# Optimization experiments

Measured on AMD Instinct MI355X. Metric: run time of the kernel, lower is better.

## Reference

```python
import jax, jax.numpy as jnp
import numpy as np

B = 32
M = 3
MAG_DIM = 20
STD = 0.28
INV = float(1.0 / (np.sqrt(2.0) * STD))
NORM = float(1.0 / (np.sqrt(2.0 * np.pi) * STD))


def _lrelu(x):
    return jax.nn.leaky_relu(x, 0.01)


def _conv(x, w, b):
    y = jax.lax.conv_general_dilated(x, w, (2, 2), 'VALID',
                                     dimension_numbers=('NCHW', 'OIHW', 'NCHW'))
    return _lrelu(y + b[None, :, None, None])


def _combos(x):
    # x: [N, c, d] -> [N, c, c, 2d], pairs[n, i, j] = concat(x[n, i], x[n, j])
    # (matches torch getCombinations: tensorB = expand-over-i, tensorA = expand-over-j)
    N, c, d = x.shape
    left = jnp.broadcast_to(x[:, :, None, :], (N, c, c, d))
    right = jnp.broadcast_to(x[:, None, :, :], (N, c, c, d))
    return jnp.concatenate([left, right], axis=-1)


def _forward(batch, conv_w1, conv_b1, conv_w2, conv_b2, conv_w3, conv_b3, conv_w4, conv_b4,
             post_w, post_b, g_w1, g_b1, g_w2, g_b2, g_w3, g_b3, g_w4, g_b4,
             h_w1, h_b1, h_w2, h_b2, h_w3, h_b3, f_w1, f_b1, f_w2, f_b2, ff_w, ff_b):
    bsz = batch.shape[0]
    x = batch.reshape(bsz * 16, 1, 80, 80)
    # magnitude encoding (computed under no_grad in the original)
    mag = jnp.linspace(-1.0, 1.0, MAG_DIM).astype(batch.dtype)  # [20]
    t = jnp.tanh(x * (2.0 / 255.0) - 1.0)                        # [N,1,80,80]
    enc = NORM * jnp.exp(-(((t + mag[None, :, None, None]) * INV) ** 2))  # [N,20,80,80]
    enc = jax.lax.stop_gradient(enc)
    y = _conv(enc, conv_w1, conv_b1)   # [N,32,39,39]
    y = _conv(y, conv_w2, conv_b2)     # [N,32,19,19]
    y = _conv(y, conv_w3, conv_b3)     # [N,32,9,9]
    y = _conv(y, conv_w4, conv_b4)     # [N,32,4,4]
    obj = y.reshape(bsz * 16, 512) @ post_w + post_b             # [N,247]
    panel = obj.reshape(bsz, 16, 247)
    given, options = panel[:, :8], panel[:, 8:]
    giv = jnp.broadcast_to(given[:, None], (bsz, 8, 8, 247))
    ctx = jnp.concatenate([giv, options[:, :, None, :]], axis=2)  # [B,8,9,247]
    tags = jnp.broadcast_to(jnp.eye(9, dtype=batch.dtype), (bsz * 8, 9, 9))
    objects = jnp.concatenate([ctx.reshape(bsz * 8, 9, 247), tags], axis=-1)  # [B*8,9,256]

    z = _combos(objects).reshape(-1, 512)  # [B*8*81, 512]
    z = _lrelu(z @ g_w1 + g_b1)
    z = _lrelu(z @ g_w2 + g_b2)
    z = _lrelu(z @ g_w3 + g_b3)
    z = _lrelu(z @ g_w4 + g_b4)
    sum_j = z.reshape(bsz * 8, 9, 9, 256).sum(axis=2)  # [B*8,9,256]
    for i in range(h_w1.shape[0]):
        p = _combos(sum_j).reshape(-1, 512)
        z = _lrelu(p @ h_w1[i] + h_b1[i])
        z = _lrelu(z @ h_w2[i] + h_b2[i])
        z = _lrelu(z @ h_w3[i] + h_b3[i])
        sum_j = z.reshape(bsz * 8, 9, 9, 256).sum(axis=2)
    h_sum = sum_j.sum(axis=1)                          # [B*8,256]
    z = _lrelu(h_sum @ f_w1 + f_b1)
    z = _lrelu(z @ f_w2 + f_b2)
    result = z @ ff_w + ff_b                           # [B*8,1]
    answer = result.reshape(bsz, 8)
    loss = jnp.mean(h_sum ** 2) + jnp.mean(result ** 2)
    return answer, loss


def setup_inputs():
    key = jax.random.key(0)
    ks = iter(jax.random.split(key, 40))

    def U(shape, fan_in):
        s = 1.0 / np.sqrt(fan_in)
        return jax.random.uniform(next(ks), shape, jnp.float32, -s, s)

    inp = {
        'batch': jax.random.uniform(next(ks), (B, 16, 80, 80), jnp.float32, 0.0, 255.0),
        'conv_w1': U((32, MAG_DIM, 3, 3), MAG_DIM * 9), 'conv_b1': U((32,), MAG_DIM * 9),
        'conv_w2': U((32, 32, 3, 3), 288), 'conv_b2': U((32,), 288),
        'conv_w3': U((32, 32, 3, 3), 288), 'conv_b3': U((32,), 288),
        'conv_w4': U((32, 32, 3, 3), 288), 'conv_b4': U((32,), 288),
        'post_w': U((512, 247), 512), 'post_b': U((247,), 512),
        'g_w1': U((512, 512), 512), 'g_b1': U((512,), 512),
        'g_w2': U((512, 512), 512), 'g_b2': U((512,), 512),
        'g_w3': U((512, 512), 512), 'g_b3': U((512,), 512),
        'g_w4': U((512, 256), 512), 'g_b4': U((256,), 512),
        'h_w1': U((M, 512, 256), 512), 'h_b1': U((M, 256), 512),
        'h_w2': U((M, 256, 256), 256), 'h_b2': U((M, 256), 256),
        'h_w3': U((M, 256, 256), 256), 'h_b3': U((M, 256), 256),
        'f_w1': U((256, 256), 256), 'f_b1': U((256,), 256),
        'f_w2': U((256, 256), 256), 'f_b2': U((256,), 256),
        'ff_w': U((256, 1), 256), 'ff_b': U((1,), 256),
    }
    return inp


def reference(batch, conv_w1, conv_b1, conv_w2, conv_b2, conv_w3, conv_b3, conv_w4, conv_b4,
              post_w, post_b, g_w1, g_b1, g_w2, g_b2, g_w3, g_b3, g_w4, g_b4,
              h_w1, h_b1, h_w2, h_b2, h_w3, h_b3, f_w1, f_b1, f_w2, f_b2, ff_w, ff_b):
    return _forward(batch, conv_w1, conv_b1, conv_w2, conv_b2, conv_w3, conv_b3, conv_w4, conv_b4,
                    post_w, post_b, g_w1, g_b1, g_w2, g_b2, g_w3, g_b3, g_w4, g_b4,
                    h_w1, h_b1, h_w2, h_b2, h_w3, h_b3, f_w1, f_b1, f_w2, f_b2, ff_w, ff_b)
```

## Files before the change

kernel.cpp:

```cpp
#include <hip/hip_runtime.h>
#include <hip/hip_bf16.h>
#include <math.h>

static __device__ __forceinline__ float lrelu(float v){ return v > 0.0f ? v : 0.01f*v; }

static __device__ __forceinline__ unsigned short f2bf(float f){
  unsigned int u = __float_as_uint(f);
  unsigned int r = (u + 0x7fffu + ((u >> 16) & 1u)) >> 16;
  return (unsigned short)r;
}
static __device__ __forceinline__ float bf2f(unsigned short u){
  return __uint_as_float(((unsigned int)u) << 16);
}
static __device__ __forceinline__ unsigned int pack_bf2(float lo, float hi){
  __hip_bfloat162 bb = __float22bfloat162_rn(make_float2(lo, hi));
  return *reinterpret_cast<unsigned int*>(&bb);
}
static __device__ __forceinline__ void gload16(const void* g, void* l){
  __builtin_amdgcn_global_load_lds(
    (const __attribute__((address_space(1))) void*)(const void*)g,
    (__attribute__((address_space(3))) void*)l, 16, 0, 0);
}

#define ENC_NORM 1.4247939f
#define GC_C     6.3775511f
#define GC_2CD   1.3426423f
#define GC_CD2   0.070665395f
#define GC_S1    0.86820227f

typedef __attribute__((ext_vector_type(4))) float f32x4;
typedef __attribute__((ext_vector_type(8))) short bf16x8;

__global__ __launch_bounds__(256) void k_prep(
    const float* __restrict__ g_w1, const float* __restrict__ g_w2,
    const float* __restrict__ g_w3, const float* __restrict__ g_w4,
    const float* __restrict__ h_w1, const float* __restrict__ h_w2,
    const float* __restrict__ h_w3, const float* __restrict__ post_w,
    const float* __restrict__ conv_w2, const float* __restrict__ conv_w3,
    const float* __restrict__ conv_w4, const float* __restrict__ conv_w1,
    const float* __restrict__ f_w1, const float* __restrict__ f_w2,
    unsigned short* __restrict__ WT)
{
  int e = blockIdx.x*256 + threadIdx.x;
  float v;
  if (e < 262144) {
    int nn = e >> 8, kk = e & 255;
    v = (nn < 512) ? g_w1[kk*512 + nn] : g_w1[(256+kk)*512 + (nn-512)];
  } else if (e < 524288) {
    int r = e - 262144; int nn = r >> 9, kk = r & 511;
    v = g_w2[kk*512 + nn];
  } else if (e < 786432) {
    int r = e - 524288; int nn = r >> 9, kk = r & 511;
    v = g_w3[kk*512 + nn];
  } else if (e < 917504) {
    int r = e - 786432; int nn = r >> 9, kk = r & 511;
    v = g_w4[kk*256 + nn];
  } else if (e < 1310720) {
    int r = e - 917504; int i = r >> 17; int q = r & 131071;
    int nn = q >> 8, kk = q & 255;
    v = (nn < 256) ? h_w1[i*131072 + kk*256 + nn]
                   : h_w1[i*131072 + (256+kk)*256 + (nn-256)];
  } else if (e < 1507328) {
    int r = e - 1310720; int i = r >> 16; int q = r & 65535;
    int nn = q >> 8, kk = q & 255;
    v = h_w2[i*65536 + kk*256 + nn];
  } else if (e < 1703936) {
    int r = e - 1507328; int i = r >> 16; int q = r & 65535;
    int nn = q >> 8, kk = q & 255;
    v = h_w3[i*65536 + kk*256 + nn];
  } else if (e < 1835008) {
    int r = e - 1703936; int np = r >> 9, kp = r & 511;
    int px = kp >> 5, c = kp & 31;
    v = (np < 247) ? post_w[(c*16+px)*247 + np] : 0.f;
  } else if (e < 1862656) {
    int r = e - 1835008; int which = r / 9216; int q = r % 9216;
    int tap = q >> 10, o = (q >> 5) & 31, c = q & 31;
    const float* w = which==0 ? conv_w2 : (which==1 ? conv_w3 : conv_w4);
    v = w[(o*32+c)*9 + tap];
  } else if (e < 1871872) {
    int r = e - 1862656; int tap = r >> 10, o = (r >> 5) & 31, c = r & 31;
    v = (c < 20) ? conv_w1[(o*20+c)*9 + tap] : 0.f;
  } else if (e < 1937408) {
    int r = e - 1871872; int nn = r >> 8, kk = r & 255;
    v = f_w1[kk*256 + nn];
  } else {
    int r = e - 1937408; int nn = r >> 8, kk = r & 255;
    v = f_w2[kk*256 + nn];
  }
  WT[e] = f2bf(v);
}

__global__ __launch_bounds__(256, 1) void k_conv1m(
    const float* __restrict__ batch, const unsigned short* __restrict__ wc1,
    const float* __restrict__ bias, unsigned short* __restrict__ y)
{
  __shared__ unsigned short ench[7][41][40];
  int n = blockIdx.x;
  int h = blockIdx.y;
  int c0 = h * 40;
  int OWH = h ? 19 : 20;
  int owbase = h * 20;
  int tid = threadIdx.x;
  int lane = tid & 63, wid = tid >> 6;
  int lr = lane & 15, kg = lane >> 4;

  bf16x8 bf0[9], bf1[9];
  #pragma unroll
  for (int tap = 0; tap < 9; ++tap) {
    bf0[tap] = *(const bf16x8*)&wc1[tap*1024 + lr*32 + kg*8];
    bf1[tap] = *(const bf16x8*)&wc1[tap*1024 + (16+lr)*32 + kg*8];
  }
  float b0 = bias[lr], b1 = bias[16 + lr];
  const float S2 = GC_S1 * GC_S1;

  for (int s = 0; s < 13; ++s) {
    int orow0 = s * 3;
    int irow0 = orow0 * 2;
    const float* img = batch + (size_t)n*6400 + irow0*80;
    for (int p = tid; p < 7*41; p += 256) {
      int row = p / 41, hx = p % 41;
      int lc = (hx < 21) ? 2*hx : 2*(hx-21)+1;
      int c = c0 + lc;
      if (c > 78) continue;
      float x = img[row*80 + c];
      float E = __expf(x * (4.0f/255.0f) - 2.0f);
      float t = 1.0f - 2.0f*__builtin_amdgcn_rcpf(E + 1.0f);
      float z = t - 1.0f;
      float e = ENC_NORM * __expf(-GC_C*z*z);
      float rg = __expf(-GC_2CD*z - GC_CD2);
      unsigned int pk[16];
      #pragma unroll
      for (int cp = 0; cp < 10; ++cp) {
        float e1 = e * rg;
        pk[cp] = pack_bf2(e, e1);
        e  = e1 * rg * GC_S1;
        rg = rg * S2;
      }
      #pragma unroll
      for (int cp = 10; cp < 16; ++cp) pk[cp] = 0u;
      unsigned short* dst = &ench[row][hx][0];
      *(uint4*)(dst)      = *(uint4*)&pk[0];
      *(uint4*)(dst + 8)  = *(uint4*)&pk[4];
      *(uint4*)(dst + 16) = *(uint4*)&pk[8];
      *(uint4*)(dst + 24) = *(uint4*)&pk[12];
    }
    __syncthreads();

    int totpx = 3 * OWH;
    {
      int t = wid;
      int pa = t*16 + lr;
      int pc = (pa < totpx) ? pa : (totpx - 1);
      int ohl = pc / OWH, lw = pc % OWH;
      f32x4 acc0 = {0.f,0.f,0.f,0.f}, acc1 = {0.f,0.f,0.f,0.f};
      #pragma unroll
      for (int kh = 0; kh < 3; ++kh) {
        int r = ohl*2 + kh;
        #pragma unroll
        for (int kw = 0; kw < 3; ++kw) {
          int hidx = (kw == 1) ? (21 + lw) : (lw + (kw >> 1));
          bf16x8 a = *(const bf16x8*)&ench[r][hidx][kg*8];
          int tap = kh*3 + kw;
          acc0 = __builtin_amdgcn_mfma_f32_16x16x32_bf16(a, bf0[tap], acc0, 0, 0, 0);
          acc1 = __builtin_amdgcn_mfma_f32_16x16x32_bf16(a, bf1[tap], acc1, 0, 0, 0);
        }
      }
      #pragma unroll
      for (int rr = 0; rr < 4; ++rr) {
        int ps = t*16 + kg*4 + rr;
        if (ps < totpx) {
          int soh = orow0 + ps / OWH, sow = owbase + ps % OWH;
          unsigned short* op = y + (((size_t)n*39 + soh)*39 + sow)*32;
          op[lr]      = f2bf(lrelu(acc0[rr] + b0));
          op[16 + lr] = f2bf(lrelu(acc1[rr] + b1));
        }
      }
    }
    __syncthreads();
  }
}

template<int H, int W, int OH, int OW, int ROWS, int SLABS>
__global__ __launch_bounds__(256, 1) void k_cmfma(
    const unsigned short* __restrict__ in, const unsigned short* __restrict__ wc,
    const float* __restrict__ bias, unsigned short* __restrict__ out)
{
  constexpr int IR = 2*ROWS + 1;
  constexpr int EV = (W + 1) / 2;
  __shared__ unsigned short xs[IR][W][40];
  int n = blockIdx.x;
  int tid = threadIdx.x;
  int lane = tid & 63, wid = tid >> 6;
  int lr = lane & 15, kg = lane >> 4;

  bf16x8 bf0[9], bf1[9];
  #pragma unroll
  for (int tap = 0; tap < 9; ++tap) {
    bf0[tap] = *(const bf16x8*)&wc[(tap*32 + lr)*32      + kg*8];
    bf1[tap] = *(const bf16x8*)&wc[(tap*32 + 16 + lr)*32 + kg*8];
  }
  float b0 = bias[lr], b1 = bias[16 + lr];

  for (int s = 0; s < SLABS; ++s) {
    int orow0 = (blockIdx.y * SLABS + s) * ROWS;
    if (orow0 >= OH) break;
    int nrows = min(ROWS, OH - orow0);
    int irow0 = orow0 * 2;
    int ir = min(2*nrows + 1, H - irow0);

    const unsigned short* ip = in + ((size_t)n*H + irow0)*W*32;
    int npx = ir * W;
    for (int p = tid; p < npx; p += 256) {
      const uint4* src = (const uint4*)(ip + (size_t)p*32);
      uint4 v0 = src[0], v1 = src[1], v2 = src[2], v3 = src[3];
      int r = p / W, col = p % W;
      int hx = (col & 1) ? EV + (col >> 1) : (col >> 1);
      unsigned short* dst = &xs[r][hx][0];
      *(uint4*)(dst)      = v0;
      *(uint4*)(dst + 8)  = v1;
      *(uint4*)(dst + 16) = v2;
      *(uint4*)(dst + 24) = v3;
    }
    __syncthreads();

    int totpx = nrows * OW;
    int ntiles = (totpx + 15) >> 4;
    for (int t = wid; t < ntiles; t += 4) {
      int pa = t*16 + lr;
      int pc = (pa < totpx) ? pa : 0;
      int oh = pc / OW, ow = pc % OW;
      f32x4 acc0 = {0.f,0.f,0.f,0.f}, acc1 = {0.f,0.f,0.f,0.f};
      #pragma unroll
      for (int kh = 0; kh < 3; ++kh)
        #pragma unroll
        for (int kw = 0; kw < 3; ++kw) {
          int hidx = (kw == 1) ? (EV + ow) : (ow + (kw >> 1));
          bf16x8 a = *(const bf16x8*)&xs[oh*2 + kh][hidx][kg*8];
          acc0 = __builtin_amdgcn_mfma_f32_16x16x32_bf16(a, bf0[kh*3+kw], acc0, 0, 0, 0);
          acc1 = __builtin_amdgcn_mfma_f32_16x16x32_bf16(a, bf1[kh*3+kw], acc1, 0, 0, 0);
        }
      #pragma unroll
      for (int rr = 0; rr < 4; ++rr) {
        int ps = t*16 + kg*4 + rr;
        if (ps < totpx) {
          int soh = orow0 + ps / OW, sow = ps % OW;
          unsigned short* op = out + (((size_t)n*OH + soh)*OW + sow)*32;
          op[lr]      = f2bf(lrelu(acc0[rr] + b0));
          op[16 + lr] = f2bf(lrelu(acc1[rr] + b1));
        }
      }
    }
    __syncthreads();
  }
}

template<int OUT_BF16, int ACT>
__global__ __launch_bounds__(256) void k_mgemm(
    const unsigned short* __restrict__ A, const unsigned short* __restrict__ Wt,
    const float* __restrict__ bias, void* __restrict__ Cv,
    int M, int N, int K)
{
  __shared__ unsigned short As[128*64];
  __shared__ unsigned short Bs[128*64];
  int bm = blockIdx.x * 128;
  int bn = blockIdx.y * 128;
  int tid = threadIdx.x;
  int wid = tid >> 6, lane = tid & 63;
  int wr = (wid >> 1) * 64, wc = (wid & 1) * 64;
  int lr = lane & 15, kg = lane >> 4;

  int srow = lane >> 3;
  int ssw  = ((lane & 7) * 16) ^ (srow << 4);
  int rsw  = (lr & 7) << 4;

  f32x4 acc[4][4];
  #pragma unroll
  for (int i = 0; i < 4; ++i)
    #pragma unroll
    for (int j = 0; j < 4; ++j)
      acc[i][j] = (f32x4){0.f,0.f,0.f,0.f};

  for (int k0 = 0; k0 < K; k0 += 64) {
    #pragma unroll
    for (int i = 0; i < 4; ++i) {
      int rowc = wid*32 + i*8;
      int row  = rowc + srow;
      gload16((const char*)&A[(size_t)(bm + row)*K + k0] + ssw, &As[rowc*64]);
      gload16((const char*)&Wt[(size_t)(bn + row)*K + k0] + ssw, &Bs[rowc*64]);
    }
    __syncthreads();
    #pragma unroll
    for (int ks = 0; ks < 2; ++ks) {
      int roff = ((ks*64 + kg*16) ^ rsw) >> 1;
      bf16x8 a[4], b[4];
      #pragma unroll
      for (int i = 0; i < 4; ++i) {
        a[i] = *(const bf16x8*)&As[(wr + i*16 + lr)*64 + roff];
        b[i] = *(const bf16x8*)&Bs[(wc + i*16 + lr)*64 + roff];
      }
      #pragma unroll
      for (int i = 0; i < 4; ++i)
        #pragma unroll
        for (int j = 0; j < 4; ++j)
          acc[i][j] = __builtin_amdgcn_mfma_f32_16x16x32_bf16(a[i], b[j], acc[i][j], 0, 0, 0);
    }
    __syncthreads();
  }
  int r0 = (lane >> 4) * 4;
  #pragma unroll
  for (int i = 0; i < 4; ++i) {
    #pragma unroll
    for (int j = 0; j < 4; ++j) {
      int col = bn + wc + j*16 + lr;
      float bv = bias ? bias[col] : 0.f;
      #pragma unroll
      for (int rr = 0; rr < 4; ++rr) {
        int row = bm + wr + i*16 + r0 + rr;
        float v = acc[i][j][rr] + bv;
        if (ACT) v = lrelu(v);
        if (OUT_BF16) ((unsigned short*)Cv)[(size_t)row*N + col] = f2bf(v);
        else          ((float*)Cv)[(size_t)row*N + col] = v;
      }
    }
  }
}

__global__ __launch_bounds__(256) void k_pgemm(
    const unsigned short* __restrict__ UV, const unsigned short* __restrict__ Wt,
    const float* __restrict__ abias, const float* __restrict__ obias,
    unsigned short* __restrict__ C, int M, int N, int K)
{
  __shared__ unsigned short As[128*64];
  __shared__ unsigned short Bs[128*64];
  __shared__ float absm[512];
  int bm = blockIdx.x * 128;
  int bn = blockIdx.y * 128;
  int tid = threadIdx.x;
  int wid = tid >> 6, lane = tid & 63;
  int wr = (wid >> 1) * 64, wc = (wid & 1) * 64;
  int lr = lane & 15, kg = lane >> 4;
  int ld = 2*K;

  int srow = lane >> 3;
  int ssw  = ((lane & 7) * 16) ^ (srow << 4);
  int rsw  = (lr & 7) << 4;

  for (int idx = tid; idx < K; idx += 256) absm[idx] = abias[idx];

  int urow[4], vrow[4], arow[4], asw[4];
  #pragma unroll
  for (int i = 0; i < 4; ++i) {
    int ch = tid + (i << 8);
    int r = ch >> 3;
    int m = bm + r;
    int n = m / 81; int rem = m - n*81;
    int ii = rem / 9; int jj = rem - ii*9;
    urow[i] = n*9 + ii; vrow[i] = n*9 + jj;
    arow[i] = r;
    asw[i] = (((ch & 7) * 16) ^ ((r & 7) << 4)) >> 1;
  }
  __syncthreads();

  f32x4 acc[4][4];
  #pragma unroll
  for (int i = 0; i < 4; ++i)
    #pragma unroll
    for (int j = 0; j < 4; ++j)
      acc[i][j] = (f32x4){0.f,0.f,0.f,0.f};

  for (int k0 = 0; k0 < K; k0 += 64) {
    #pragma unroll
    for (int i = 0; i < 4; ++i) {
      int rowc = wid*32 + i*8;
      int row  = rowc + srow;
      gload16((const char*)&Wt[(size_t)(bn + row)*K + k0] + ssw, &Bs[rowc*64]);
    }
    #pragma unroll
    for (int i = 0; i < 4; ++i) {
      int ch = tid + (i << 8);
      int kc = (ch & 7) * 8;
      uint4 u4 = *(const uint4*)&UV[(size_t)urow[i]*ld + k0 + kc];
      uint4 v4 = *(const uint4*)&UV[(size_t)vrow[i]*ld + K + k0 + kc];
      const unsigned short* us = (const unsigned short*)&u4;
      const unsigned short* vs = (const unsigned short*)&v4;
      unsigned int pk[4];
      #pragma unroll
      for (int e2 = 0; e2 < 4; ++e2) {
        float a0 = bf2f(us[2*e2])   + bf2f(vs[2*e2])   + absm[k0 + kc + 2*e2];
        float a1 = bf2f(us[2*e2+1]) + bf2f(vs[2*e2+1]) + absm[k0 + kc + 2*e2+1];
        pk[e2] = pack_bf2(lrelu(a0), lrelu(a1));
      }
      *(uint4*)&As[arow[i]*64 + asw[i]] = *(uint4*)pk;
    }
    __syncthreads();
    #pragma unroll
    for (int ks = 0; ks < 2; ++ks) {
      int roff = ((ks*64 + kg*16) ^ rsw) >> 1;
      bf16x8 a[4], b[4];
      #pragma unroll
      for (int i = 0; i < 4; ++i) {
        a[i] = *(const bf16x8*)&As[(wr + i*16 + lr)*64 + roff];
        b[i] = *(const bf16x8*)&Bs[(wc + i*16 + lr)*64 + roff];
      }
      #pragma unroll
      for (int i = 0; i < 4; ++i)
        #pragma unroll
        for (int j = 0; j < 4; ++j)
          acc[i][j] = __builtin_amdgcn_mfma_f32_16x16x32_bf16(a[i], b[j], acc[i][j], 0, 0, 0);
    }
    __syncthreads();
  }
  int r0 = (lane >> 4) * 4;
  #pragma unroll
  for (int i = 0; i < 4; ++i) {
    #pragma unroll
    for (int j = 0; j < 4; ++j) {
      int col = bn + wc + j*16 + lr;
      float bv = obias[col];
      #pragma unroll
      for (int rr = 0; rr < 4; ++rr) {
        int row = bm + wr + i*16 + r0 + rr;
        C[(size_t)row*N + col] = f2bf(lrelu(acc[i][j][rr] + bv));
      }
    }
  }
}

__global__ void k_objects(const float* __restrict__ panel, const float* __restrict__ post_b,
                          unsigned short* __restrict__ obj)
{
  int idx = blockIdx.x*256 + threadIdx.x;
  int row = idx >> 8;
  int k = idx & 255;
  int slot = row % 9;
  int nn = row / 9;
  int b = nn >> 3, opt = nn & 7;
  float v;
  if (k < 247) {
    int src = (slot < 8) ? (b*16 + slot) : (b*16 + 8 + opt);
    v = panel[(size_t)src*256 + k] + post_b[k];
  } else {
    v = ((k - 247) == slot) ? 1.0f : 0.0f;
  }
  obj[idx] = f2bf(v);
}

__global__ void k_sumj(const unsigned short* __restrict__ Z, float* __restrict__ SJ,
                       unsigned short* __restrict__ SJb, int C)
{
  int idx = blockIdx.x*256 + threadIdx.x;
  int vpr = C >> 3;
  int orow = idx / vpr, kv = (idx - orow*vpr) << 3;
  int n = orow / 9, i = orow % 9;
  const unsigned short* base = Z + (size_t)(n*81 + i*9)*C + kv;
  float s[8];
  #pragma unroll
  for (int e = 0; e < 8; ++e) s[e] = 0.f;
  #pragma unroll
  for (int j = 0; j < 9; ++j) {
    bf16x8 v = *(const bf16x8*)(base + (size_t)j*C);
    #pragma unroll
    for (int e = 0; e < 8; ++e) s[e] += bf2f(((const unsigned short*)&v)[e]);
  }
  float* so = SJ + (size_t)orow*C + kv;
  #pragma unroll
  for (int e = 0; e < 8; ++e) so[e] = s[e];
  unsigned int pk[4];
  #pragma unroll
  for (int e2 = 0; e2 < 4; ++e2) pk[e2] = pack_bf2(s[2*e2], s[2*e2+1]);
  *(uint4*)(SJb + (size_t)orow*C + kv) = *(uint4*)pk;
}

__global__ void k_hsum(const float* __restrict__ SJ, float* __restrict__ HS,
                       unsigned short* __restrict__ HSb)
{
  int idx = blockIdx.x*256 + threadIdx.x;
  int n = idx >> 6, kc = (idx & 63) << 2;
  const float* base = SJ + (size_t)n*9*256 + kc;
  float4 s = {0.f,0.f,0.f,0.f};
  #pragma unroll
  for (int i = 0; i < 9; ++i) {
    float4 v = *(const float4*)(base + (size_t)i*256);
    s.x += v.x; s.y += v.y; s.z += v.z; s.w += v.w;
  }
  *(float4*)(HS + (size_t)n*256 + kc) = s;
  unsigned int pk[2];
  pk[0] = pack_bf2(s.x, s.y);
  pk[1] = pack_bf2(s.z, s.w);
  *(uint2*)(HSb + (size_t)n*256 + kc) = *(uint2*)pk;
}

__global__ __launch_bounds__(256) void k_tailfin(
    const float* __restrict__ HS, const unsigned short* __restrict__ F2,
    const float* __restrict__ ffw, const float* __restrict__ ffb,
    float* __restrict__ out)
{
  __shared__ float red[256];
  __shared__ float wsm[256];
  int tid = threadIdx.x;
  wsm[tid] = ffw[tid];
  float s = 0.f;
  for (int j = 0; j < 256; ++j) { float v = HS[j*256 + tid]; s += v*v; }
  red[tid] = s; __syncthreads();
  for (int off = 128; off > 0; off >>= 1) { if (tid < off) red[tid] += red[tid + off]; __syncthreads(); }
  float hsq = red[0];
  __syncthreads();
  float r = ffb[0];
  for (int k = 0; k < 256; ++k) r += bf2f(F2[(size_t)tid*256 + k])*wsm[k];
  red[tid] = r*r; __syncthreads();
  for (int off = 128; off > 0; off >>= 1) { if (tid < off) red[tid] += red[tid + off]; __syncthreads(); }
  out[tid] = r;
  if (tid == 0) out[256] = hsq/65536.0f + red[0]/256.0f;
}

extern "C" void kernel_launch(void* const* d_in, const int* in_sizes, int n_in,
                              void* d_out, int out_size, void* d_ws, size_t ws_size,
                              hipStream_t stream)
{
  const float* batch   = (const float*)d_in[0];
  const float* conv_w1 = (const float*)d_in[1];
  const float* conv_b1 = (const float*)d_in[2];
  const float* conv_w2 = (const float*)d_in[3];
  const float* conv_b2 = (const float*)d_in[4];
  const float* conv_w3 = (const float*)d_in[5];
  const float* conv_b3 = (const float*)d_in[6];
  const float* conv_w4 = (const float*)d_in[7];
  const float* conv_b4 = (const float*)d_in[8];
  const float* post_w  = (const float*)d_in[9];
  const float* post_b  = (const float*)d_in[10];
  const float* g_w1    = (const float*)d_in[11];
  const float* g_b1    = (const float*)d_in[12];
  const float* g_w2    = (const float*)d_in[13];
  const float* g_b2    = (const float*)d_in[14];
  const float* g_w3    = (const float*)d_in[15];
  const float* g_b3    = (const float*)d_in[16];
  const float* g_w4    = (const float*)d_in[17];
  const float* g_b4    = (const float*)d_in[18];
  const float* h_w1    = (const float*)d_in[19];
  const float* h_b1    = (const float*)d_in[20];
  const float* h_w2    = (const float*)d_in[21];
  const float* h_b2    = (const float*)d_in[22];
  const float* h_w3    = (const float*)d_in[23];
  const float* h_b3    = (const float*)d_in[24];
  const float* f_w1    = (const float*)d_in[25];
  const float* f_b1    = (const float*)d_in[26];
  const float* f_w2    = (const float*)d_in[27];
  const float* f_b2    = (const float*)d_in[28];
  const float* ff_w    = (const float*)d_in[29];
  const float* ff_b    = (const float*)d_in[30];

  char* wsb = (char*)d_ws;
  const size_t off_Y1    = 0;
  const size_t off_Y2    = 52000000;
  const size_t off_Y3    = 64000000;
  const size_t off_Y4    = 67000000;
  const size_t off_PANEL = 68000000;
  const size_t off_WT    = 132000000;
  const size_t off_Pb    = 0;
  const size_t off_Qb    = 22000000;
  const size_t off_UV    = 44000000;
  const size_t off_OBJb  = 54000000;
  const size_t off_SJ    = 56000000;
  const size_t off_SJb   = 59000000;
  const size_t off_HS    = 61000000;
  const size_t off_HSb   = 61500000;
  const size_t off_F1    = 62000000;
  const size_t off_F2    = 63000000;

  unsigned short* WT = (unsigned short*)(wsb + off_WT);
  const size_t wt_g1   = 0;
  const size_t wt_g2   = 262144;
  const size_t wt_g3   = 524288;
  const size_t wt_g4   = 786432;
  const size_t wt_h1   = 917504;
  const size_t wt_h2   = 1310720;
  const size_t wt_h3   = 1507328;
  const size_t wt_post = 1703936;
  const size_t wt_cw2  = 1835008;
  const size_t wt_cw3  = 1844224;
  const size_t wt_cw4  = 1853440;
  const size_t wt_cw1  = 1862656;
  const size_t wt_f1   = 1871872;
  const size_t wt_f2   = 1937408;

  dim3 b256(256);

  k_prep<<<dim3(7824), b256, 0, stream>>>(g_w1, g_w2, g_w3, g_w4, h_w1, h_w2, h_w3,
                                          post_w, conv_w2, conv_w3, conv_w4, conv_w1,
                                          f_w1, f_w2, WT);

  unsigned short* Y1 = (unsigned short*)(wsb + off_Y1);
  unsigned short* Y2 = (unsigned short*)(wsb + off_Y2);
  unsigned short* Y3 = (unsigned short*)(wsb + off_Y3);
  unsigned short* Y4 = (unsigned short*)(wsb + off_Y4);
  float* PANEL = (float*)(wsb + off_PANEL);

  k_conv1m<<<dim3(512,2), b256, 0, stream>>>(batch, WT + wt_cw1, conv_b1, Y1);
  k_cmfma<39,39,19,19, 5,2><<<dim3(512,2), b256, 0, stream>>>(Y1, WT + wt_cw2, conv_b2, Y2);
  k_cmfma<19,19, 9, 9, 9,1><<<dim3(512,1), b256, 0, stream>>>(Y2, WT + wt_cw3, conv_b3, Y3);
  k_cmfma< 9, 9, 4, 4, 4,1><<<dim3(512,1), b256, 0, stream>>>(Y3, WT + wt_cw4, conv_b4, Y4);

  k_mgemm<0,0><<<dim3(4,2), b256, 0, stream>>>(Y4, WT + wt_post, nullptr, PANEL, 512,256,512);

  unsigned short* OBJb = (unsigned short*)(wsb + off_OBJb);
  unsigned short* Pb   = (unsigned short*)(wsb + off_Pb);
  unsigned short* Qb   = (unsigned short*)(wsb + off_Qb);
  unsigned short* SJb  = (unsigned short*)(wsb + off_SJb);
  unsigned short* UVb  = (unsigned short*)(wsb + off_UV);
  float* SJ = (float*)(wsb + off_SJ);
  float* HS = (float*)(wsb + off_HS);
  unsigned short* HSb = (unsigned short*)(wsb + off_HSb);
  unsigned short* F1 = (unsigned short*)(wsb + off_F1);
  unsigned short* F2 = (unsigned short*)(wsb + off_F2);

  k_objects<<<dim3(2304), b256, 0, stream>>>(PANEL, post_b, OBJb);

  k_mgemm<1,0><<<dim3(18,8), b256, 0, stream>>>(OBJb, WT + wt_g1, nullptr, UVb, 2304,1024,256);
  k_pgemm<<<dim3(162,4), b256, 0, stream>>>(UVb, WT + wt_g2, g_b1, g_b2, Qb, 20736,512,512);
  k_mgemm<1,1><<<dim3(162,4), b256, 0, stream>>>(Qb, WT + wt_g3, g_b3, Pb, 20736,512,512);
  k_mgemm<1,1><<<dim3(162,2), b256, 0, stream>>>(Pb, WT + wt_g4, g_b4, Qb, 20736,256,512);
  k_sumj<<<dim3(288), b256, 0, stream>>>(Qb, SJ, SJb, 256);

  for (int i = 0; i < 3; ++i) {
    k_mgemm<1,0><<<dim3(18,4), b256, 0, stream>>>(SJb, WT + wt_h1 + (size_t)i*131072, nullptr, UVb, 2304,512,256);
    k_pgemm<<<dim3(162,2), b256, 0, stream>>>(UVb, WT + wt_h2 + (size_t)i*65536, h_b1 + i*256, h_b2 + i*256, Qb, 20736,256,256);
    k_mgemm<1,1><<<dim3(162,2), b256, 0, stream>>>(Qb, WT + wt_h3 + (size_t)i*65536, h_b3 + i*256, Pb, 20736,256,256);
    k_sumj<<<dim3(288), b256, 0, stream>>>(Pb, SJ, SJb, 256);
  }

  k_hsum<<<dim3(64), b256, 0, stream>>>(SJ, HS, HSb);
  k_mgemm<1,1><<<dim3(2,2), b256, 0, stream>>>(HSb, WT + wt_f1, f_b1, F1, 256,256,256);
  k_mgemm<1,1><<<dim3(2,2), b256, 0, stream>>>(F1,  WT + wt_f2, f_b2, F2, 256,256,256);
  k_tailfin<<<dim3(1), b256, 0, stream>>>(HS, F2, ff_w, ff_b, (float*)d_out);
}
```

Before: 340.4 us.

## Fuse small reduction/prep kernels into GEMM loaders and merge conv3/conv4

```diff
diff --git a/kernel.cpp b/kernel.cpp
--- a/kernel.cpp
+++ b/kernel.cpp
@@ -100,6 +100,8 @@
   int c0 = h * 40;
   int OWH = h ? 19 : 20;
   int owbase = h * 20;
+  int s0 = blockIdx.z * 7;
+  int s1 = blockIdx.z ? 13 : 7;
   int tid = threadIdx.x;
   int lane = tid & 63, wid = tid >> 6;
   int lr = lane & 15, kg = lane >> 4;
@@ -113,7 +115,7 @@
   float b0 = bias[lr], b1 = bias[16 + lr];
   const float S2 = GC_S1 * GC_S1;
 
-  for (int s = 0; s < 13; ++s) {
+  for (int s = s0; s < s1; ++s) {
     int orow0 = s * 3;
     int irow0 = orow0 * 2;
     const float* img = batch + (size_t)n*6400 + irow0*80;
@@ -254,6 +256,95 @@
   }
 }
 
+__global__ __launch_bounds__(256, 1) void k_conv34(
+    const unsigned short* __restrict__ in,
+    const unsigned short* __restrict__ wc3, const float* __restrict__ b3,
+    const unsigned short* __restrict__ wc4, const float* __restrict__ b4,
+    unsigned short* __restrict__ out)
+{
+  __shared__ unsigned short xs[19][19][40];
+  __shared__ unsigned short ys[9][9][40];
+  int n = blockIdx.x;
+  int tid = threadIdx.x;
+  int lane = tid & 63, wid = tid >> 6;
+  int lr = lane & 15, kg = lane >> 4;
+
+  bf16x8 c3a[9], c3b[9], c4a[9], c4b[9];
+  #pragma unroll
+  for (int tap = 0; tap < 9; ++tap) {
+    c3a[tap] = *(const bf16x8*)&wc3[(tap*32 + lr)*32      + kg*8];
+    c3b[tap] = *(const bf16x8*)&wc3[(tap*32 + 16 + lr)*32 + kg*8];
+    c4a[tap] = *(const bf16x8*)&wc4[(tap*32 + lr)*32      + kg*8];
+    c4b[tap] = *(const bf16x8*)&wc4[(tap*32 + 16 + lr)*32 + kg*8];
+  }
+  float b30 = b3[lr], b31 = b3[16+lr];
+  float b40 = b4[lr], b41 = b4[16+lr];
+
+  const unsigned short* ip = in + (size_t)n*19*19*32;
+  for (int p = tid; p < 361; p += 256) {
+    const uint4* src = (const uint4*)(ip + (size_t)p*32);
+    uint4 v0 = src[0], v1 = src[1], v2 = src[2], v3 = src[3];
+    int r = p / 19, col = p % 19;
+    int hx = (col & 1) ? 10 + (col >> 1) : (col >> 1);
+    unsigned short* dst = &xs[r][hx][0];
+    *(uint4*)(dst)      = v0;
+    *(uint4*)(dst + 8)  = v1;
+    *(uint4*)(dst + 16) = v2;
+    *(uint4*)(dst + 24) = v3;
+  }
+  __syncthreads();
+
+  for (int t = wid; t < 6; t += 4) {
+    int pa = t*16 + lr;
+    int pc = (pa < 81) ? pa : 0;
+    int oh = pc / 9, ow = pc % 9;
+    f32x4 acc0 = {0.f,0.f,0.f,0.f}, acc1 = {0.f,0.f,0.f,0.f};
+    #pragma unroll
+    for (int kh = 0; kh < 3; ++kh)
+      #pragma unroll
+      for (int kw = 0; kw < 3; ++kw) {
+        int hidx = (kw == 1) ? (10 + ow) : (ow + (kw >> 1));
+        bf16x8 a = *(const bf16x8*)&xs[oh*2 + kh][hidx][kg*8];
+        acc0 = __builtin_amdgcn_mfma_f32_16x16x32_bf16(a, c3a[kh*3+kw], acc0, 0, 0, 0);
+        acc1 = __builtin_amdgcn_mfma_f32_16x16x32_bf16(a, c3b[kh*3+kw], acc1, 0, 0, 0);
+      }
+    #pragma unroll
+    for (int rr = 0; rr < 4; ++rr) {
+      int ps = t*16 + kg*4 + rr;
+      if (ps < 81) {
+        int soh = ps / 9, sow = ps % 9;
+        int hx2 = (sow & 1) ? 5 + (sow >> 1) : (sow >> 1);
+        ys[soh][hx2][lr]      = f2bf(lrelu(acc0[rr] + b30));
+        ys[soh][hx2][16 + lr] = f2bf(lrelu(acc1[rr] + b31));
+      }
+    }
+  }
+  __syncthreads();
+
+  if (wid == 0) {
+    int pc = lr;
+    int oh = pc >> 2, ow = pc & 3;
+    f32x4 acc0 = {0.f,0.f,0.f,0.f}, acc1 = {0.f,0.f,0.f,0.f};
+    #pragma unroll
+    for (int kh = 0; kh < 3; ++kh)
+      #pragma unroll
+      for (int kw = 0; kw < 3; ++kw) {
+        int hidx = (kw == 1) ? (5 + ow) : (ow + (kw >> 1));
+        bf16x8 a = *(const bf16x8*)&ys[oh*2 + kh][hidx][kg*8];
+        acc0 = __builtin_amdgcn_mfma_f32_16x16x32_bf16(a, c4a[kh*3+kw], acc0, 0, 0, 0);
+        acc1 = __builtin_amdgcn_mfma_f32_16x16x32_bf16(a, c4b[kh*3+kw], acc1, 0, 0, 0);
+      }
+    #pragma unroll
+    for (int rr = 0; rr < 4; ++rr) {
+      int ps = kg*4 + rr;
+      int soh = ps >> 2, sow = ps & 3;
+      unsigned short* op = out + (((size_t)n*4 + soh)*4 + sow)*32;
+      op[lr]      = f2bf(lrelu(acc0[rr] + b40));
+      op[16 + lr] = f2bf(lrelu(acc1[rr] + b41));
+    }
+  }
+}
+
 template<int OUT_BF16, int ACT>
 __global__ __launch_bounds__(256) void k_mgemm(
     const unsigned short* __restrict__ A, const unsigned short* __restrict__ Wt,
@@ -426,87 +517,384 @@
   }
 }
 
-__global__ void k_objects(const float* __restrict__ panel, const float* __restrict__ post_b,
-                          unsigned short* __restrict__ obj)
+__global__ __launch_bounds__(256) void k_g1o(
+    const float* __restrict__ panel, const float* __restrict__ post_b,
+    const unsigned short* __restrict__ Wt, unsigned short* __restrict__ C,
+    int M, int N, int K)
 {
-  int idx = blockIdx.x*256 + threadIdx.x;
-  int row = idx >> 8;
-  int k = idx & 255;
-  int slot = row % 9;
-  int nn = row / 9;
-  int b = nn >> 3, opt = nn & 7;
-  float v;
-  if (k < 247) {
-    int src = (slot < 8) ? (b*16 + slot) : (b*16 + 8 + opt);
-    v = panel[(size_t)src*256 + k] + post_b[k];
-  } else {
-    v = ((k - 247) == slot) ? 1.0f : 0.0f;
-  }
-  obj[idx] = f2bf(v);
-}
-
-__global__ void k_sumj(const unsigned short* __restrict__ Z, float* __restrict__ SJ,
-                       unsigned short* __restrict__ SJb, int C)
+  __shared__ unsigned short As[128*64];
+  __shared__ unsigned short Bs[128*64];
+  __shared__ float pbs[256];
+  int bm = blockIdx.x * 128;
+  int bn = blockIdx.y * 128;
+  int tid = threadIdx.x;
+  int wid = tid >> 6, lane = tid & 63;
+  int wr = (wid >> 1) * 64, wc = (wid & 1) * 64;
+  int lr = lane & 15, kg = lane >> 4;
+
+  int srow = lane >> 3;
+  int ssw  = ((lane & 7) * 16) ^ (srow << 4);
+  int rsw  = (lr & 7) << 4;
+
+  if (tid < 256) pbs[tid] = (tid < 247) ? post_b[tid] : 0.f;
+
+  int srcr[4], slotr[4], arow[4], asw[4];
+  #pragma unroll
+  for (int i = 0; i < 4; ++i) {
+    int ch = tid + (i << 8);
+    int r = ch >> 3;
+    int m = bm + r;
+    int nn = m / 9; int sl = m - nn*9;
+    int b = nn >> 3, opt = nn & 7;
+    srcr[i] = (sl < 8) ? (b*16 + sl) : (b*16 + 8 + opt);
+    slotr[i] = sl;
+    arow[i] = r;
+    asw[i] = (((ch & 7) * 16) ^ ((r & 7) << 4)) >> 1;
+  }
+  __syncthreads();
+
+  f32x4 acc[4][4];
+  #pragma unroll
+  for (int i = 0; i < 4; ++i)
+    #pragma unroll
+    for (int j = 0; j < 4; ++j)
+      acc[i][j] = (f32x4){0.f,0.f,0.f,0.f};
+
+  for (int k0 = 0; k0 < K; k0 += 64) {
+    #pragma unroll
+    for (int i = 0; i < 4; ++i) {
+      int rowc = wid*32 + i*8;
+      int row  = rowc + srow;
+      gload16((const char*)&Wt[(size_t)(bn + row)*K + k0] + ssw, &Bs[rowc*64]);
+    }
+    #pragma unroll
+    for (int i = 0; i < 4; ++i) {
+      int ch = tid + (i << 8);
+      int kc = (ch & 7) * 8;
+      int kb = k0 + kc;
+      const float* pp = &panel[(size_t)srcr[i]*256 + kb];
+      unsigned int pk[4];
+      #pragma unroll
+      for (int e2 = 0; e2 < 4; ++e2) {
+        float v0 = pp[2*e2]   + pbs[kb + 2*e2];
+        float v1 = pp[2*e2+1] + pbs[kb + 2*e2+1];
+        int kk0 = kb + 2*e2, kk1 = kb + 2*e2 + 1;
+        if (kk0 >= 247) v0 = (kk0 - 247 == slotr[i]) ? 1.f : 0.f;
+        if (kk1 >= 247) v1 = (kk1 - 247 == slotr[i]) ? 1.f : 0.f;
+        pk[e2] = pack_bf2(v0, v1);
+      }
+      *(uint4*)&As[arow[i]*64 + asw[i]] = *(uint4*)pk;
+    }
+    __syncthreads();
+    #pragma unroll
+    for (int ks = 0; ks < 2; ++ks) {
+      int roff = ((ks*64 + kg*16) ^ rsw) >> 1;
+      bf16x8 a[4], b[4];
+      #pragma unroll
+      for (int i = 0; i < 4; ++i) {
+        a[i] = *(const bf16x8*)&As[(wr + i*16 + lr)*64 + roff];
+        b[i] = *(const bf16x8*)&Bs[(wc + i*16 + lr)*64 + roff];
+      }
+      #pragma unroll
+      for (int i = 0; i < 4; ++i)
+        #pragma unroll
+        for (int j = 0; j < 4; ++j)
+          acc[i][j] = __builtin_amdgcn_mfma_f32_16x16x32_bf16(a[i], b[j], acc[i][j], 0, 0, 0);
+    }
+    __syncthreads();
+  }
+  int r0 = (lane >> 4) * 4;
+  #pragma unroll
+  for (int i = 0; i < 4; ++i) {
+    #pragma unroll
+    for (int j = 0; j < 4; ++j) {
+      int col = bn + wc + j*16 + lr;
+      #pragma unroll
+      for (int rr = 0; rr < 4; ++rr) {
+        int row = bm + wr + i*16 + r0 + rr;
+        C[(size_t)row*N + col] = f2bf(acc[i][j][rr]);
+      }
+    }
+  }
+}
+
+__global__ __launch_bounds__(256) void k_h1s(
+    const unsigned short* __restrict__ Z, const unsigned short* __restrict__ Wt,
+    unsigned short* __restrict__ C, int M, int N, int K)
 {
-  int idx = blockIdx.x*256 + threadIdx.x;
-  int vpr = C >> 3;
-  int orow = idx / vpr, kv = (idx - orow*vpr) << 3;
-  int n = orow / 9, i = orow % 9;
-  const unsigned short* base = Z + (size_t)(n*81 + i*9)*C + kv;
-  float s[8];
-  #pragma unroll
-  for (int e = 0; e < 8; ++e) s[e] = 0.f;
-  #pragma unroll
-  for (int j = 0; j < 9; ++j) {
-    bf16x8 v = *(const bf16x8*)(base + (size_t)j*C);
-    #pragma unroll
-    for (int e = 0; e < 8; ++e) s[e] += bf2f(((const unsigned short*)&v)[e]);
-  }
-  float* so = SJ + (size_t)orow*C + kv;
-  #pragma unroll
-  for (int e = 0; e < 8; ++e) so[e] = s[e];
-  unsigned int pk[4];
-  #pragma unroll
-  for (int e2 = 0; e2 < 4; ++e2) pk[e2] = pack_bf2(s[2*e2], s[2*e2+1]);
-  *(uint4*)(SJb + (size_t)orow*C + kv) = *(uint4*)pk;
-}
-
-__global__ void k_hsum(const float* __restrict__ SJ, float* __restrict__ HS,
-                       unsigned short* __restrict__ HSb)
+  __shared__ unsigned short As[128*64];
+  __shared__ unsigned short Bs[128*64];
+  int bm = blockIdx.x * 128;
+  int bn = blockIdx.y * 128;
+  int tid = threadIdx.x;
+  int wid = tid >> 6, lane = tid & 63;
+  int wr = (wid >> 1) * 64, wc = (wid & 1) * 64;
+  int lr = lane & 15, kg = lane >> 4;
+
+  int srow = lane >> 3;
+  int ssw  = ((lane & 7) * 16) ^ (srow << 4);
+  int rsw  = (lr & 7) << 4;
+
+  int arow[4], asw[4];
+  #pragma unroll
+  for (int i = 0; i < 4; ++i) {
+    int ch = tid + (i << 8);
+    int r = ch >> 3;
+    arow[i] = r;
+    asw[i] = (((ch & 7) * 16) ^ ((r & 7) << 4)) >> 1;
+  }
+
+  f32x4 acc[4][4];
+  #pragma unroll
+  for (int i = 0; i < 4; ++i)
+    #pragma unroll
+    for (int j = 0; j < 4; ++j)
+      acc[i][j] = (f32x4){0.f,0.f,0.f,0.f};
+
+  for (int k0 = 0; k0 < K; k0 += 64) {
+    #pragma unroll
+    for (int i = 0; i < 4; ++i) {
+      int rowc = wid*32 + i*8;
+      int row  = rowc + srow;
+      gload16((const char*)&Wt[(size_t)(bn + row)*K + k0] + ssw, &Bs[rowc*64]);
+    }
+    #pragma unroll
+    for (int i = 0; i < 4; ++i) {
+      int ch = tid + (i << 8);
+      int kc = (ch & 7) * 8;
+      const unsigned short* zp = Z + (size_t)(bm + arow[i])*9*256 + k0 + kc;
+      float s[8];
+      #pragma unroll
+      for (int e = 0; e < 8; ++e) s[e] = 0.f;
+      #pragma unroll
+      for (int j = 0; j < 9; ++j) {
+        bf16x8 v = *(const bf16x8*)(zp + (size_t)j*256);
+        #pragma unroll
+        for (int e = 0; e < 8; ++e) s[e] += bf2f(((const unsigned short*)&v)[e]);
+      }
+      unsigned int pk[4];
+      #pragma unroll
+      for (int e2 = 0; e2 < 4; ++e2) pk[e2] = pack_bf2(s[2*e2], s[2*e2+1]);
+      *(uint4*)&As[arow[i]*64 + asw[i]] = *(uint4*)pk;
+    }
+    __syncthreads();
+    #pragma unroll
+    for (int ks = 0; ks < 2; ++ks) {
+      int roff = ((ks*64 + kg*16) ^ rsw) >> 1;
+      bf16x8 a[4], b[4];
+      #pragma unroll
+      for (int i = 0; i < 4; ++i) {
+        a[i] = *(const bf16x8*)&As[(wr + i*16 + lr)*64 + roff];
+        b[i] = *(const bf16x8*)&Bs[(wc + i*16 + lr)*64 + roff];
+      }
+      #pragma unroll
+      for (int i = 0; i < 4; ++i)
+        #pragma unroll
+        for (int j = 0; j < 4; ++j)
+          acc[i][j] = __builtin_amdgcn_mfma_f32_16x16x32_bf16(a[i], b[j], acc[i][j], 0, 0, 0);
+    }
+    __syncthreads();
+  }
+  int r0 = (lane >> 4) * 4;
+  #pragma unroll
+  for (int i = 0; i < 4; ++i) {
+    #pragma unroll
+    for (int j = 0; j < 4; ++j) {
+      int col = bn + wc + j*16 + lr;
+      #pragma unroll
+      for (int rr = 0; rr < 4; ++rr) {
+        int row = bm + wr + i*16 + r0 + rr;
+        C[(size_t)row*N + col] = f2bf(acc[i][j][rr]);
+      }
+    }
+  }
+}
+
+__global__ __launch_bounds__(256) void k_head1(
+    const unsigned short* __restrict__ Z, const unsigned short* __restrict__ Wt,
+    const float* __restrict__ bias, unsigned short* __restrict__ F1,
+    float* __restrict__ HS)
 {
-  int idx = blockIdx.x*256 + threadIdx.x;
-  int n = idx >> 6, kc = (idx & 63) << 2;
-  const float* base = SJ + (size_t)n*9*256 + kc;
-  float4 s = {0.f,0.f,0.f,0.f};
-  #pragma unroll
-  for (int i = 0; i < 9; ++i) {
-    float4 v = *(const float4*)(base + (size_t)i*256);
-    s.x += v.x; s.y += v.y; s.z += v.z; s.w += v.w;
-  }
-  *(float4*)(HS + (size_t)n*256 + kc) = s;
-  unsigned int pk[2];
-  pk[0] = pack_bf2(s.x, s.y);
-  pk[1] = pack_bf2(s.z, s.w);
-  *(uint2*)(HSb + (size_t)n*256 + kc) = *(uint2*)pk;
-}
-
-__global__ __launch_bounds__(256) void k_tailfin(
-    const float* __restrict__ HS, const unsigned short* __restrict__ F2,
-    const float* __restrict__ ffw, const float* __restrict__ ffb,
+  __shared__ unsigned short As[128*64];
+  __shared__ unsigned short Bs[128*64];
+  int bm = blockIdx.x * 128;
+  int bn = blockIdx.y * 128;
+  int tid = threadIdx.x;
+  int wid = tid >> 6, lane = tid & 63;
+  int wr = (wid >> 1) * 64, wc = (wid & 1) * 64;
+  int lr = lane & 15, kg = lane >> 4;
+
+  int srow = lane >> 3;
+  int ssw  = ((lane & 7) * 16) ^ (srow << 4);
+  int rsw  = (lr & 7) << 4;
+
+  int arow[4], asw[4];
+  #pragma unroll
+  for (int i = 0; i < 4; ++i) {
+    int ch = tid + (i << 8);
+    int r = ch >> 3;
+    arow[i] = r;
+    asw[i] = (((ch & 7) * 16) ^ ((r & 7) << 4)) >> 1;
+  }
+
+  f32x4 acc[4][4];
+  #pragma unroll
+  for (int i = 0; i < 4; ++i)
+    #pragma unroll
+    for (int j = 0; j < 4; ++j)
+      acc[i][j] = (f32x4){0.f,0.f,0.f,0.f};
+
+  for (int k0 = 0; k0 < 256; k0 += 64) {
+    #pragma unroll
+    for (int i = 0; i < 4; ++i) {
+      int rowc = wid*32 + i*8;
+      int row  = rowc + srow;
+      gload16((const char*)&Wt[(size_t)(bn + row)*256 + k0] + ssw, &Bs[rowc*64]);
+    }
+    #pragma unroll
+    for (int i = 0; i < 4; ++i) {
+      int ch = tid + (i << 8);
+      int kc = (ch & 7) * 8;
+      const unsigned short* zp = Z + (size_t)(bm + arow[i])*81*256 + k0 + kc;
+      float s[8];
+      #pragma unroll
+      for (int e = 0; e < 8; ++e) s[e] = 0.f;
+      for (int q = 0; q < 81; ++q) {
+        bf16x8 v = *(const bf16x8*)(zp + (size_t)q*256);
+        #pragma unroll
+        for (int e = 0; e < 8; ++e) s[e] += bf2f(((const unsigned short*)&v)[e]);
+      }
+      if (blockIdx.y == 0) {
+        float* hp = HS + (size_t)(bm + arow[i])*256 + k0 + kc;
+        *(float4*)hp       = (float4){s[0],s[1],s[2],s[3]};
+        *(float4*)(hp + 4) = (float4){s[4],s[5],s[6],s[7]};
+      }
+      unsigned int pk[4];
+      #pragma unroll
+      for (int e2 = 0; e2 < 4; ++e2) pk[e2] = pack_bf2(s[2*e2], s[2*e2+1]);
+      *(uint4*)&As[arow[i]*64 + asw[i]] = *(uint4*)pk;
+    }
+    __syncthreads();
+    #pragma unroll
+    for (int ks = 0; ks < 2; ++ks) {
+      int roff = ((ks*64 + kg*16) ^ rsw) >> 1;
+      bf16x8 a[4], b[4];
+      #pragma unroll
+      for (int i = 0; i < 4; ++i) {
+        a[i] = *(const bf16x8*)&As[(wr + i*16 + lr)*64 + roff];
+        b[i] = *(const bf16x8*)&Bs[(wc + i*16 + lr)*64 + roff];
+      }
+      #pragma unroll
+      for (int i = 0; i < 4; ++i)
+        #pragma unroll
+        for (int j = 0; j < 4; ++j)
+          acc[i][j] = __builtin_amdgcn_mfma_f32_16x16x32_bf16(a[i], b[j], acc[i][j], 0, 0, 0);
+    }
+    __syncthreads();
+  }
+  int r0 = (lane >> 4) * 4;
+  #pragma unroll
+  for (int i = 0; i < 4; ++i) {
+    #pragma unroll
+    for (int j = 0; j < 4; ++j) {
+      int col = bn + wc + j*16 + lr;
+      float bv = bias[col];
+      #pragma unroll
+      for (int rr = 0; rr < 4; ++rr) {
+        int row = bm + wr + i*16 + r0 + rr;
+        F1[(size_t)row*256 + col] = f2bf(lrelu(acc[i][j][rr] + bv));
+      }
+    }
+  }
+}
+
+__global__ __launch_bounds__(256) void k_head2(
+    const unsigned short* __restrict__ F1, const unsigned short* __restrict__ Wt,
+    const float* __restrict__ f_b2, const float* __restrict__ ffw,
+    const float* __restrict__ ffb, const float* __restrict__ HS,
     float* __restrict__ out)
 {
-  __shared__ float red[256];
-  __shared__ float wsm[256];
+  __shared__ unsigned short As[128*64];
+  __shared__ unsigned short Bs[128*64];
+  __shared__ float wsm[256], bsm[256], resf[256], red[256];
   int tid = threadIdx.x;
+  int wid = tid >> 6, lane = tid & 63;
+  int wr = (wid >> 1) * 64, wc = (wid & 1) * 64;
+  int lr = lane & 15, kg = lane >> 4;
+
+  int srow = lane >> 3;
+  int ssw  = ((lane & 7) * 16) ^ (srow << 4);
+  int rsw  = (lr & 7) << 4;
+
   wsm[tid] = ffw[tid];
-  float s = 0.f;
-  for (int j = 0; j < 256; ++j) { float v = HS[j*256 + tid]; s += v*v; }
-  red[tid] = s; __syncthreads();
+  bsm[tid] = f_b2[tid];
+  resf[tid] = 0.f;
+  __syncthreads();
+
+  for (int bm = 0; bm < 256; bm += 128)
+  for (int bn = 0; bn < 256; bn += 128) {
+    f32x4 acc[4][4];
+    #pragma unroll
+    for (int i = 0; i < 4; ++i)
+      #pragma unroll
+      for (int j = 0; j < 4; ++j)
+        acc[i][j] = (f32x4){0.f,0.f,0.f,0.f};
+
+    for (int k0 = 0; k0 < 256; k0 += 64) {
+      #pragma unroll
+      for (int i = 0; i < 4; ++i) {
+        int rowc = wid*32 + i*8;
+        int row  = rowc + srow;
+        gload16((const char*)&F1[(size_t)(bm + row)*256 + k0] + ssw, &As[rowc*64]);
+        gload16((const char*)&Wt[(size_t)(bn + row)*256 + k0] + ssw, &Bs[rowc*64]);
+      }
+      __syncthreads();
+      #pragma unroll
+      for (int ks = 0; ks < 2; ++ks) {
+        int roff = ((ks*64 + kg*16) ^ rsw) >> 1;
+        bf16x8 a[4], b[4];
+        #pragma unroll
+        for (int i = 0; i < 4; ++i) {
+          a[i] = *(const bf16x8*)&As[(wr + i*16 + lr)*64 + roff];
+          b[i] = *(const bf16x8*)&Bs[(wc + i*16 + lr)*64 + roff];
+        }
+        #pragma unroll
+        for (int i = 0; i < 4; ++i)
+          #pragma unroll
+          for (int j = 0; j < 4; ++j)
+            acc[i][j] = __builtin_amdgcn_mfma_f32_16x16x32_bf16(a[i], b[j], acc[i][j], 0, 0, 0);
+      }
+      __syncthreads();
+    }
+    int r0 = (lane >> 4) * 4;
+    #pragma unroll
+    for (int i = 0; i < 4; ++i) {
+      #pragma unroll
+      for (int rr = 0; rr < 4; ++rr) {
+        float s = 0.f;
+        #pragma unroll
+        for (int j = 0; j < 4; ++j) {
+          int col = bn + wc + j*16 + lr;
+          float v = lrelu(acc[i][j][rr] + bsm[col]);
+          s += v * wsm[col];
+        }
+        s += __shfl_xor(s, 1);
+        s += __shfl_xor(s, 2);
+        s += __shfl_xor(s, 4);
+        s += __shfl_xor(s, 8);
+        if ((lane & 15) == 0)
+          atomicAdd(&resf[bm + wr + i*16 + r0 + rr], s);
+      }
+    }
+    __syncthreads();
+  }
+  float sq = 0.f;
+  for (int j = 0; j < 256; ++j) { float v = HS[j*256 + tid]; sq += v*v; }
+  red[tid] = sq; __syncthreads();
   for (int off = 128; off > 0; off >>= 1) { if (tid < off) red[tid] += red[tid + off]; __syncthreads(); }
   float hsq = red[0];
   __syncthreads();
-  float r = ffb[0];
-  for (int k = 0; k < 256; ++k) r += bf2f(F2[(size_t)tid*256 + k])*wsm[k];
+  float r = resf[tid] + ffb[0];
   red[tid] = r*r; __syncthreads();
   for (int off = 128; off > 0; off >>= 1) { if (tid < off) red[tid] += red[tid + off]; __syncthreads(); }
   out[tid] = r;
@@ -552,20 +940,14 @@
   char* wsb = (char*)d_ws;
   const size_t off_Y1    = 0;
   const size_t off_Y2    = 52000000;
-  const size_t off_Y3    = 64000000;
   const size_t off_Y4    = 67000000;
   const size_t off_PANEL = 68000000;
   const size_t off_WT    = 132000000;
   const size_t off_Pb    = 0;
   const size_t off_Qb    = 22000000;
   const size_t off_UV    = 44000000;
-  const size_t off_OBJb  = 54000000;
-  const size_t off_SJ    = 56000000;
-  const size_t off_SJb   = 59000000;
   const size_t off_HS    = 61000000;
-  const size_t off_HSb   = 61500000;
   const size_t off_F1    = 62000000;
-  const size_t off_F2    = 63000000;
 
   unsigned short* WT = (unsigned short*)(wsb + off_WT);
   const size_t wt_g1   = 0;
@@ -591,45 +973,34 @@
 
   unsigned short* Y1 = (unsigned short*)(wsb + off_Y1);
   unsigned short* Y2 = (unsigned short*)(wsb + off_Y2);
-  unsigned short* Y3 = (unsigned short*)(wsb + off_Y3);
   unsigned short* Y4 = (unsigned short*)(wsb + off_Y4);
   float* PANEL = (float*)(wsb + off_PANEL);
 
-  k_conv1m<<<dim3(512,2), b256, 0, stream>>>(batch, WT + wt_cw1, conv_b1, Y1);
-  k_cmfma<39,39,19,19, 5,2><<<dim3(512,2), b256, 0, stream>>>(Y1, WT + wt_cw2, conv_b2, Y2);
-  k_cmfma<19,19, 9, 9, 9,1><<<dim3(512,1), b256, 0, stream>>>(Y2, WT + wt_cw3, conv_b3, Y3);
-  k_cmfma< 9, 9, 4, 4, 4,1><<<dim3(512,1), b256, 0, stream>>>(Y3, WT + wt_cw4, conv_b4, Y4);
+  k_conv1m<<<dim3(512,2,2), b256, 0, stream>>>(batch, WT + wt_cw1, conv_b1, Y1);
+  k_cmfma<39,39,19,19,5,2><<<dim3(512,2), b256, 0, stream>>>(Y1, WT + wt_cw2, conv_b2, Y2);
+  k_conv34<<<dim3(512), b256, 0, stream>>>(Y2, WT + wt_cw3, conv_b3, WT + wt_cw4, conv_b4, Y4);
 
   k_mgemm<0,0><<<dim3(4,2), b256, 0, stream>>>(Y4, WT + wt_post, nullptr, PANEL, 512,256,512);
 
-  unsigned short* OBJb = (unsigned short*)(wsb + off_OBJb);
-  unsigned short* Pb   = (unsigned short*)(wsb + off_Pb);
-  unsigned short* Qb   = (unsigned short*)(wsb + off_Qb);
-  unsigned short* SJb  = (unsigned short*)(wsb + off_SJb);
-  unsigned short* UVb  = (unsigned short*)(wsb + off_UV);
-  float* SJ = (float*)(wsb + off_SJ);
+  unsigned short* Pb  = (unsigned short*)(wsb + off_Pb);
+  unsigned short* Qb  = (unsigned short*)(wsb + off_Qb);
+  unsigned short* UVb = (unsigned short*)(wsb + off_UV);
   float* HS = (float*)(wsb + off_HS);
-  unsigned short* HSb = (unsigned short*)(wsb + off_HSb);
   unsigned short* F1 = (unsigned short*)(wsb + off_F1);
-  unsigned short* F2 = (unsigned short*)(wsb + off_F2);
-
-  k_objects<<<dim3(2304), b256, 0, stream>>>(PANEL, post_b, OBJb);
-
-  k_mgemm<1,0><<<dim3(18,8), b256, 0, stream>>>(OBJb, WT + wt_g1, nullptr, UVb, 2304,1024,256);
+
+  k_g1o<<<dim3(18,8), b256, 0, stream>>>(PANEL, post_b, WT + wt_g1, UVb, 2304,1024,256);
   k_pgemm<<<dim3(162,4), b256, 0, stream>>>(UVb, WT + wt_g2, g_b1, g_b2, Qb, 20736,512,512);
   k_mgemm<1,1><<<dim3(162,4), b256, 0, stream>>>(Qb, WT + wt_g3, g_b3, Pb, 20736,512,512);
   k_mgemm<1,1><<<dim3(162,2), b256, 0, stream>>>(Pb, WT + wt_g4, g_b4, Qb, 20736,256,512);
-  k_sumj<<<dim3(288), b256, 0, stream>>>(Qb, SJ, SJb, 256);
-
+
+  const unsigned short* Zprev = Qb;
   for (int i = 0; i < 3; ++i) {
-    k_mgemm<1,0><<<dim3(18,4), b256, 0, stream>>>(SJb, WT + wt_h1 + (size_t)i*131072, nullptr, UVb, 2304,512,256);
+    k_h1s<<<dim3(18,4), b256, 0, stream>>>(Zprev, WT + wt_h1 + (size_t)i*131072, UVb, 2304,512,256);
     k_pgemm<<<dim3(162,2), b256, 0, stream>>>(UVb, WT + wt_h2 + (size_t)i*65536, h_b1 + i*256, h_b2 + i*256, Qb, 20736,256,256);
     k_mgemm<1,1><<<dim3(162,2), b256, 0, stream>>>(Qb, WT + wt_h3 + (size_t)i*65536, h_b3 + i*256, Pb, 20736,256,256);
-    k_sumj<<<dim3(288), b256, 0, stream>>>(Pb, SJ, SJb, 256);
-  }
-
-  k_hsum<<<dim3(64), b256, 0, stream>>>(SJ, HS, HSb);
-  k_mgemm<1,1><<<dim3(2,2), b256, 0, stream>>>(HSb, WT + wt_f1, f_b1, F1, 256,256,256);
-  k_mgemm<1,1><<<dim3(2,2), b256, 0, stream>>>(F1,  WT + wt_f2, f_b2, F2, 256,256,256);
-  k_tailfin<<<dim3(1), b256, 0, stream>>>(HS, F2, ff_w, ff_b, (float*)d_out);
-}
+    Zprev = Pb;
+  }
+
+  k_head1<<<dim3(2,2), b256, 0, stream>>>(Pb, WT + wt_f1, f_b1, F1, HS);
+  k_head2<<<dim3(1), b256, 0, stream>>>(F1, WT + wt_f2, f_b2, ff_w, ff_b, HS, (float*)d_out);
+}
```

After: 609.7 us. +79.1%, slower.
